# Kernel optimization log

Measured on AMD Instinct MI355X. Metric: run time of the kernel, lower is better.

Reference implementation:

```python
import jax, jax.numpy as jnp
import numpy as np

B, L, D, H, R = 4, 4096, 1024, 16, 30
DK = D // H  # 64
EPS = 1e-12  # torch F.normalize eps


def setup_inputs() -> dict:
    key = jax.random.key(0)
    ks = jax.random.split(key, 16)
    n = lambda k, shp, s=0.02: jax.random.normal(k, shp, jnp.float32) * s
    return {
        "queries": jax.random.normal(ks[0], (B, L, D), jnp.float32),
        "keys": jax.random.normal(ks[1], (B, L, D), jnp.float32),
        "values": jax.random.normal(ks[2], (B, L, D), jnp.float32),
        # linear weights stored as (in, out); equivalent to torch y = x @ W.T + b
        "Wq": n(ks[3], (D, D)), "bq": jnp.zeros((D,), jnp.float32),
        "Wk": n(ks[4], (D, D)), "bk": jnp.zeros((D,), jnp.float32),
        "We": n(ks[5], (H, DK, R), 0.1),
        "Wr": n(ks[6], (H, DK, R), 0.1),
        "Lam": jax.random.uniform(ks[7], (H, R), jnp.float32),
        "Wc": n(ks[8], (2 * R, DK)), "bc": jnp.zeros((DK,), jnp.float32),
        "Wo": n(ks[9], (D, D)), "bo": jnp.zeros((D,), jnp.float32),
    }


def _l2norm(x):
    nrm = jnp.sqrt(jnp.sum(x * x, axis=-1, keepdims=True))
    return x / jnp.maximum(nrm, EPS)


def reference(queries, keys, values, Wq, bq, Wk, bk, We, Wr, Lam, Wc, bc, Wo, bo):
    b, l, _ = queries.shape
    # projections -> [B, H, L, DK]
    q = (queries @ Wq + bq).reshape(b, l, H, DK).transpose(0, 2, 1, 3)
    k = (keys @ Wk + bk).reshape(b, l, H, DK).transpose(0, 2, 1, 3)
    # causal cumulative mean over sequence
    normal = (jnp.arange(l, dtype=jnp.float32) + 1.0)[None, None, :, None]
    q = jnp.cumsum(q, axis=2) / normal
    k = jnp.cumsum(k, axis=2) / normal
    # L2-normalized feature map
    q = _l2norm(q)
    k = _l2norm(k)
    # per-head low-rank projections -> [B, H, L, R]
    escore = jnp.einsum('bhld,hdr->bhlr', q, We)
    rscore = jnp.einsum('bhld,hdr->bhlr', k, Wr)
    score = jnp.concatenate([escore, rscore], axis=-1)  # [B, H, L, 2R]
    out = score @ Wc + bc                                # [B, H, L, DK]
    out = out.transpose(0, 2, 1, 3).reshape(b, l, H * DK)
    out = out @ Wo + bo                                  # [B, L, D]
    # dropout is identity in eval mode
    return (out, escore, rscore, Lam)
```

## Files before the change

### kernel.cpp

```cpp
#include <hip/hip_runtime.h>
#include <hip/hip_bf16.h>

#define BATCH 4
#define LSEQ 4096
#define DMODEL 1024
#define NHEAD 16
#define RDIM 30
#define DKH 64
#define NCHUNK 32
#define CHUNK 128

typedef __attribute__((ext_vector_type(8))) short bf16x8_t;
typedef __attribute__((ext_vector_type(4))) float f32x4_t;

static __device__ __forceinline__ unsigned short f2bf(float f) {
    __hip_bfloat16 h = __float2bfloat16(f);
    unsigned short u;
    __builtin_memcpy(&u, &h, 2);
    return u;
}
static __device__ __forceinline__ float b2f(unsigned short u) {
    unsigned v = ((unsigned)u) << 16;
    float f;
    __builtin_memcpy(&f, &v, 4);
    return f;
}

#define SWAIT_VM8()   { asm volatile("s_waitcnt vmcnt(8)" ::: "memory"); __builtin_amdgcn_sched_barrier(0); }
#define SWAIT_VM0()   { asm volatile("s_waitcnt vmcnt(0)" ::: "memory"); __builtin_amdgcn_sched_barrier(0); }
#define SWAIT_LGKM0() { asm volatile("s_waitcnt lgkmcnt(0)" ::: "memory"); __builtin_amdgcn_sched_barrier(0); }
#define SBARRIER()    { __builtin_amdgcn_s_barrier(); __builtin_amdgcn_sched_barrier(0); }

__global__ void cvt_bf16_kernel(const float* __restrict__ in, unsigned short* __restrict__ out, int n4) {
    int i = blockIdx.x * blockDim.x + threadIdx.x;
    int stride = gridDim.x * blockDim.x;
    for (; i < n4; i += stride) {
        float4 v = ((const float4*)in)[i];
        ushort4 o;
        o.x = f2bf(v.x); o.y = f2bf(v.y); o.z = f2bf(v.z); o.w = f2bf(v.w);
        ((ushort4*)out)[i] = o;
    }
}

__global__ void transpose_cvt_kernel(const float* __restrict__ W, unsigned short* __restrict__ outT,
                                     int Kd, int Nd) {
    __shared__ float tile[32][33];
    int n0 = blockIdx.x * 32, k0 = blockIdx.y * 32;
    int tx = threadIdx.x, ty = threadIdx.y;
    #pragma unroll
    for (int r = ty; r < 32; r += 8)
        tile[r][tx] = W[(size_t)(k0 + r) * Nd + n0 + tx];
    __syncthreads();
    #pragma unroll
    for (int r = ty; r < 32; r += 8)
        outT[(size_t)(n0 + r) * Kd + k0 + tx] = f2bf(tile[tx][r]);
}

__global__ void wpack_kernel(const float* __restrict__ We, const float* __restrict__ Wr,
                             unsigned short* __restrict__ WeP, unsigned short* __restrict__ WrP) {
    int h = blockIdx.x;
    const float* W = blockIdx.y ? Wr : We;
    unsigned short* O = blockIdx.y ? WrP : WeP;
    for (int idx = threadIdx.x; idx < 2048; idx += 256) {
        int col = idx >> 6, k = idx & 63;
        float v = (col < RDIM) ? W[((size_t)h * 64 + k) * RDIM + col] : 0.f;
        O[((size_t)h << 11) + idx] = f2bf(v);
    }
}

__global__ __launch_bounds__(256) void wfold_kernel(
    const float* __restrict__ Wc, const float* __restrict__ Wo,
    unsigned short* __restrict__ WfoldT)
{
    __shared__ float WoT[64][65];
    __shared__ float WcT[64][61];
    const int tid = threadIdx.x;
    const int n0 = blockIdx.x * 64, h = blockIdx.y;
    for (int i = tid; i < 4096; i += 256) {
        int dk = i >> 6, n = i & 63;
        WoT[dk][n] = Wo[(size_t)(h * 64 + dk) * DMODEL + n0 + n];
    }
    for (int i = tid; i < 3840; i += 256) {
        int j = i >> 6, dk = i & 63;
        WcT[dk][j] = Wc[j * 64 + dk];
    }
    __syncthreads();
    #pragma unroll 1
    for (int oo = 0; oo < 16; ++oo) {
        int n = (tid >> 6) + oo * 4;
        int j = tid & 63;
        int jr = (j < 30) ? j : (j >= 32 && j < 62) ? (j - 2) : -1;
        float acc = 0.f;
        if (jr >= 0) {
            #pragma unroll
            for (int dk = 0; dk < 64; ++dk)
                acc = fmaf(WcT[dk][jr], WoT[dk][n], acc);
        }
        WfoldT[(size_t)(n0 + n) * 1024 + h * 64 + j] = f2bf(acc);
    }
}

__global__ void bias2_kernel(const float* __restrict__ Wo, const float* __restrict__ bc,
                             const float* __restrict__ bo, float* __restrict__ bias2) {
    int n = blockIdx.x * 256 + threadIdx.x;
    float a = bo[n];
    for (int d = 0; d < DMODEL; ++d)
        a = fmaf(bc[d & 63], Wo[(size_t)d * DMODEL + n], a);
    bias2[n] = a;
}

#define GBM 256
#define GBN 256
#define GBK 64
#define NTILES 16

template <bool BF16_OUT>
__global__ __launch_bounds__(512, 2) void gemm8_kernel(
    const unsigned short* __restrict__ A,
    const unsigned short* __restrict__ Bt,
    const float* __restrict__ bias,
    void* __restrict__ Cv,
    int M, int N)
{
    __shared__ __align__(16) unsigned short As[2][GBM * GBK];
    __shared__ __align__(16) unsigned short Bs[2][GBM * GBK];
    const int tid = threadIdx.x;
    const int lane = tid & 63;
    const int wid = tid >> 6;
    const int wm = wid >> 2;
    const int wn = wid & 3;
    const int lm = lane & 15;
    const int kb = lane >> 4;

    const int nwg = gridDim.x * gridDim.y;
    const int wg = blockIdx.y * gridDim.x + blockIdx.x;
    const int cpx = nwg >> 3;
    const int swz = (wg & 7) * cpx + (wg >> 3);
    const int bn = swz % gridDim.x;
    const int bm = swz / gridDim.x;

    const unsigned short* Atile = A + (size_t)(bm * GBM) * 1024;
    const unsigned short* Btile = Bt + (size_t)(bn * GBN) * 1024;

    f32x4_t acc[8][4];
    #pragma unroll
    for (int i = 0; i < 8; ++i)
        #pragma unroll
        for (int j = 0; j < 4; ++j)
            acc[i][j] = f32x4_t{0.f, 0.f, 0.f, 0.f};

    auto STAGE = [&](int buf, int kt) {
        #pragma unroll
        for (int seg = 0; seg < 4; ++seg) {
            const int s = (seg << 13) + (tid << 4);
            const int row = s >> 7;
            const int cc = ((s >> 4) & 7) ^ (row & 7);
            const unsigned short* ga = Atile + (size_t)row * 1024 + kt * GBK + cc * 8;
            __builtin_amdgcn_global_load_lds(
                (const __attribute__((address_space(1))) void*)ga,
                (__attribute__((address_space(3))) void*)((char*)&As[buf][0] + (seg << 13) + (wid << 10)),
                16, 0, 0);
            const unsigned short* gb = Btile + (size_t)row * 1024 + kt * GBK + cc * 8;
            __builtin_amdgcn_global_load_lds(
                (const __attribute__((address_space(1))) void*)gb,
                (__attribute__((address_space(3))) void*)((char*)&Bs[buf][0] + (seg << 13) + (wid << 10)),
                16, 0, 0);
        }
    };

    bf16x8_t af[8], bfr[4];
    auto LOADFRAGS = [&](int buf, int ks) {
        #pragma unroll
        for (int i = 0; i < 8; ++i) {
            int row = wm * 128 + i * 16 + lm;
            int cc = (ks * 4 + kb) ^ (row & 7);
            af[i] = *(const bf16x8_t*)((const char*)&As[buf][0] + row * 128 + cc * 16);
        }
        #pragma unroll
        for (int j = 0; j < 4; ++j) {
            int row = wn * 64 + j * 16 + lm;
            int cc = (ks * 4 + kb) ^ (row & 7);
            bfr[j] = *(const bf16x8_t*)((const char*)&Bs[buf][0] + row * 128 + cc * 16);
        }
    };
    auto MFMAC = [&]() {
        __builtin_amdgcn_s_setprio(1);
        #pragma unroll
        for (int i = 0; i < 8; ++i)
            #pragma unroll
            for (int j = 0; j < 4; ++j)
                acc[i][j] = __builtin_amdgcn_mfma_f32_16x16x32_bf16(af[i], bfr[j], acc[i][j], 0, 0, 0);
        __builtin_amdgcn_s_setprio(0);
    };

    STAGE(0, 0);
    STAGE(1, 1);
    SWAIT_VM8();
    SBARRIER();

    int cur = 0;
    for (int t = 0; t < NTILES; ++t) {
        LOADFRAGS(cur, 0);
        MFMAC();
        LOADFRAGS(cur, 1);
        SWAIT_LGKM0();
        SBARRIER();
        if (t + 2 < NTILES) STAGE(cur, t + 2);
        MFMAC();
        if (t + 1 < NTILES) {
            if (t + 2 < NTILES) { SWAIT_VM8(); }
            else                { SWAIT_VM0(); }
            SBARRIER();
        }
        cur ^= 1;
    }

    #pragma unroll
    for (int i = 0; i < 8; ++i) {
        int row = bm * GBM + wm * 128 + i * 16 + (lane >> 4) * 4;
        #pragma unroll
        for (int j = 0; j < 4; ++j) {
            int col = bn * GBN + wn * 64 + j * 16 + lm;
            float bv = bias[col];
            #pragma unroll
            for (int r = 0; r < 4; ++r) {
                float v = acc[i][j][r] + bv;
                if constexpr (BF16_OUT)
                    ((unsigned short*)Cv)[(size_t)(row + r) * N + col] = f2bf(v);
                else
                    ((float*)Cv)[(size_t)(row + r) * N + col] = v;
            }
        }
    }
}

__global__ __launch_bounds__(256) void cumsum_local_kernel(
    unsigned short* __restrict__ Qb, unsigned short* __restrict__ Kb,
    float* __restrict__ partQ, float* __restrict__ partK)
{
    const int tid = threadIdx.x;
    const int c = blockIdx.x;
    const int bz = blockIdx.y;
    const int b = bz >> 1;
    unsigned short* buf = (bz & 1) ? Kb : Qb;
    float* part = (bz & 1) ? partK : partQ;
    size_t base = ((size_t)(b * LSEQ + c * CHUNK)) * DMODEL + tid * 4;
    float rx = 0.f, ry = 0.f, rz = 0.f, rw = 0.f;
    #pragma unroll 4
    for (int i = 0; i < CHUNK; ++i) {
        ushort4 v = *(ushort4*)(buf + base + (size_t)i * DMODEL);
        rx += b2f(v.x); ry += b2f(v.y); rz += b2f(v.z); rw += b2f(v.w);
        ushort4 o;
        o.x = f2bf(rx); o.y = f2bf(ry); o.z = f2bf(rz); o.w = f2bf(rw);
        *(ushort4*)(buf + base + (size_t)i * DMODEL) = o;
    }
    float4 p = make_float4(rx, ry, rz, rw);
    *(float4*)(part + ((size_t)(b * NCHUNK + c)) * DMODEL + tid * 4) = p;
}

__global__ void chunk_offsets_kernel(float* __restrict__ partQ, float* __restrict__ partK)
{
    int t = blockIdx.x * 256 + threadIdx.x;
    float* part = blockIdx.y ? partK : partQ;
    int b = t >> 10, d = t & 1023;
    float run = 0.f;
    #pragma unroll
    for (int c = 0; c < NCHUNK; ++c) {
        size_t idx = ((size_t)(b * NCHUNK + c)) * DMODEL + d;
        float v = part[idx];
        part[idx] = run;
        run += v;
    }
}

__global__ __launch_bounds__(256) void score_kernel(
    const unsigned short* __restrict__ Qc, const unsigned short* __restrict__ Kc,
    const float* __restrict__ partQ, const float* __restrict__ partK,
    const unsigned short* __restrict__ WeP, const unsigned short* __restrict__ WrP,
    float* __restrict__ escore, float* __restrict__ rscore,
    unsigned short* __restrict__ sbf)
{
    __shared__ float n2buf[4][64];
    const int tid = threadIdx.x;
    const int lane = tid & 63;
    const int w = tid >> 6;
    const int lm = lane & 15;
    const int lk = lane >> 4;
    const int c = blockIdx.x;
    const int bh = blockIdx.y;
    const int z = blockIdx.z;
    const int b = bh >> 4, h = bh & 15;
    const unsigned short* X = z ? Kc : Qc;
    const float* part = z ? partK : partQ;
    const unsigned short* WP = z ? WrP : WeP;
    float* eout = z ? rscore : escore;
    const int row0 = c * 256 + w * 64;
    const int co = c * 2 + (w >> 1);

    const float* offp = part + ((size_t)(b * NCHUNK + co)) * DMODEL + h * 64 + lk * 8;
    float o0[8], o1[8];
    {
        float4 a = *(const float4*)(offp);
        float4 bb = *(const float4*)(offp + 4);
        float4 cc = *(const float4*)(offp + 32);
        float4 dd = *(const float4*)(offp + 36);
        o0[0] = a.x; o0[1] = a.y; o0[2] = a.z; o0[3] = a.w;
        o0[4] = bb.x; o0[5] = bb.y; o0[6] = bb.z; o0[7] = bb.w;
        o1[0] = cc.x; o1[1] = cc.y; o1[2] = cc.z; o1[3] = cc.w;
        o1[4] = dd.x; o1[5] = dd.y; o1[6] = dd.z; o1[7] = dd.w;
    }

    const unsigned short* wpb = WP + ((size_t)h << 11) + lm * 64 + lk * 8;
    bf16x8_t b00 = *(const bf16x8_t*)(wpb);
    bf16x8_t b01 = *(const bf16x8_t*)(wpb + 32);
    bf16x8_t b10 = *(const bf16x8_t*)(wpb + 16 * 64);
    bf16x8_t b11 = *(const bf16x8_t*)(wpb + 16 * 64 + 32);

    f32x4_t acc[4][2];
    float n2p[4];
    #pragma unroll
    for (int i = 0; i < 4; ++i) {
        n2p[i] = 0.f;
        acc[i][0] = f32x4_t{0.f, 0.f, 0.f, 0.f};
        acc[i][1] = f32x4_t{0.f, 0.f, 0.f, 0.f};
    }

    const unsigned short* xbase = X + ((size_t)(b * LSEQ + row0 + lm)) * DMODEL + h * 64 + lk * 8;
    #pragma unroll
    for (int i = 0; i < 4; ++i) {
        const unsigned short* xp = xbase + (size_t)(16 * i) * DMODEL;
        bf16x8_t x0 = *(const bf16x8_t*)(xp);
        bf16x8_t x1 = *(const bf16x8_t*)(xp + 32);
        bf16x8_t xa0, xa1;
        #pragma unroll
        for (int j = 0; j < 8; ++j) {
            float xf = b2f((unsigned short)x0[j]) + o0[j];
            n2p[i] = fmaf(xf, xf, n2p[i]);
            xa0[j] = (short)f2bf(xf);
        }
        #pragma unroll
        for (int j = 0; j < 8; ++j) {
            float xf = b2f((unsigned short)x1[j]) + o1[j];
            n2p[i] = fmaf(xf, xf, n2p[i]);
            xa1[j] = (short)f2bf(xf);
        }
        acc[i][0] = __builtin_amdgcn_mfma_f32_16x16x32_bf16(xa0, b00, acc[i][0], 0, 0, 0);
        acc[i][1] = __builtin_amdgcn_mfma_f32_16x16x32_bf16(xa0, b10, acc[i][1], 0, 0, 0);
        acc[i][0] = __builtin_amdgcn_mfma_f32_16x16x32_bf16(xa1, b01, acc[i][0], 0, 0, 0);
        acc[i][1] = __builtin_amdgcn_mfma_f32_16x16x32_bf16(xa1, b11, acc[i][1], 0, 0, 0);
    }

    #pragma unroll
    for (int i = 0; i < 4; ++i) {
        n2p[i] += __shfl_xor(n2p[i], 16);
        n2p[i] += __shfl_xor(n2p[i], 32);
    }
    if (lane < 16) {
        #pragma unroll
        for (int i = 0; i < 4; ++i) n2buf[w][16 * i + lane] = n2p[i];
    }
    __syncthreads();

    #pragma unroll
    for (int i = 0; i < 4; ++i) {
        f32x4_t n2v = *(const f32x4_t*)&n2buf[w][16 * i + lk * 4];
        float inv[4];
        #pragma unroll
        for (int r = 0; r < 4; ++r) {
            int lr = row0 + 16 * i + lk * 4 + r;
            inv[r] = 1.f / fmaxf(sqrtf(n2v[r]), 1e-12f * (float)(lr + 1));
        }
        #pragma unroll
        for (int j = 0; j < 2; ++j) {
            int col = 16 * j + lm;
            #pragma unroll
            for (int r = 0; r < 4; ++r) {
                int lr = row0 + 16 * i + lk * 4 + r;
                float v = acc[i][j][r] * inv[r];
                if (col < RDIM)
                    eout[(((size_t)(b * NHEAD + h)) * LSEQ + lr) * RDIM + col] = v;
                sbf[((size_t)(b * LSEQ + lr)) * 1024 + h * 64 + z * 32 + col] =
                    (col < RDIM) ? f2bf(v) : (unsigned short)0;
            }
        }
    }
}

extern "C" void kernel_launch(void* const* d_in, const int* in_sizes, int n_in,
                              void* d_out, int out_size, void* d_ws, size_t ws_size,
                              hipStream_t stream)
{
    const float* queries = (const float*)d_in[0];
    const float* keys    = (const float*)d_in[1];
    const float* Wq = (const float*)d_in[3];
    const float* bq = (const float*)d_in[4];
    const float* Wk = (const float*)d_in[5];
    const float* bk = (const float*)d_in[6];
    const float* We = (const float*)d_in[7];
    const float* Wr = (const float*)d_in[8];
    const float* Lam = (const float*)d_in[9];
    const float* Wc = (const float*)d_in[10];
    const float* bc = (const float*)d_in[11];
    const float* Wo = (const float*)d_in[12];
    const float* bo = (const float*)d_in[13];

    float* out = (float*)d_out;
    float* escore = out + (size_t)16777216;
    float* rscore = out + (size_t)24641536;
    float* lam_out = out + (size_t)32505856;

    char* ws = (char*)d_ws;
    unsigned short* tmp = (unsigned short*)ws;
    unsigned short* Qb  = (unsigned short*)(ws + 33554432);
    unsigned short* Kb  = (unsigned short*)(ws + 67108864);
    unsigned short* WqT = (unsigned short*)(ws + 100663296);
    unsigned short* WkT = (unsigned short*)(ws + 102760448);
    unsigned short* WfT = (unsigned short*)(ws + 104857600);
    float* bias2 = (float*)(ws + 106954752);
    float* partQ = (float*)(ws + 106958848);
    float* partK = (float*)(ws + 107483136);
    unsigned short* WeP = (unsigned short*)(ws + 108007424);
    unsigned short* WrP = (unsigned short*)(ws + 108072960);

    const int NELEM4 = 16777216 / 4;

    dim3 tb(32, 8);
    transpose_cvt_kernel<<<dim3(32, 32), tb, 0, stream>>>(Wq, WqT, DMODEL, DMODEL);
    transpose_cvt_kernel<<<dim3(32, 32), tb, 0, stream>>>(Wk, WkT, DMODEL, DMODEL);
    wpack_kernel<<<dim3(16, 2), 256, 0, stream>>>(We, Wr, WeP, WrP);
    wfold_kernel<<<dim3(16, 16), 256, 0, stream>>>(Wc, Wo, WfT);
    bias2_kernel<<<4, 256, 0, stream>>>(Wo, bc, bo, bias2);

    cvt_bf16_kernel<<<2048, 256, 0, stream>>>(queries, tmp, NELEM4);
    gemm8_kernel<true><<<dim3(4, 64), 512, 0, stream>>>(tmp, WqT, bq, Qb, 16384, 1024);
    cvt_bf16_kernel<<<2048, 256, 0, stream>>>(keys, tmp, NELEM4);
    gemm8_kernel<true><<<dim3(4, 64), 512, 0, stream>>>(tmp, WkT, bk, Kb, 16384, 1024);

    cumsum_local_kernel<<<dim3(NCHUNK, 8), 256, 0, stream>>>(Qb, Kb, partQ, partK);
    chunk_offsets_kernel<<<dim3(16, 2), 256, 0, stream>>>(partQ, partK);

    score_kernel<<<dim3(16, 64, 2), 256, 0, stream>>>(Qb, Kb, partQ, partK, WeP, WrP,
                                                      escore, rscore, tmp);

    gemm8_kernel<false><<<dim3(4, 64), 512, 0, stream>>>(tmp, WfT, bias2, out, 16384, 1024);

    hipMemcpyAsync(lam_out, Lam, 480 * sizeof(float), hipMemcpyDeviceToDevice, stream);
}
```

Measured before the change: 282.7 us.

## Fuse fp32-to-bf16 conversion into Q/K projection GEMM and batch both via grid z

Removes the standalone cvt_bf16 kernels. The projection GEMM now loads fp32 activations into registers, converts them to bf16 and writes them into the swizzled LDS tile, with the register load software-pipelined one tile ahead. The Q and K projections are merged into a single launch using blockIdx.z. This drops a full bf16 round-trip through HBM and two launches, at the cost of reading A in fp32 (twice the bytes), higher register pressure and VALU conversion work inside the GEMM loop.

```diff
diff --git a/kernel.cpp b/kernel.cpp
--- a/kernel.cpp
+++ b/kernel.cpp
@@ -27,20 +27,10 @@
 }
 
 #define SWAIT_VM8()   { asm volatile("s_waitcnt vmcnt(8)" ::: "memory"); __builtin_amdgcn_sched_barrier(0); }
+#define SWAIT_VM4()   { asm volatile("s_waitcnt vmcnt(4)" ::: "memory"); __builtin_amdgcn_sched_barrier(0); }
 #define SWAIT_VM0()   { asm volatile("s_waitcnt vmcnt(0)" ::: "memory"); __builtin_amdgcn_sched_barrier(0); }
 #define SWAIT_LGKM0() { asm volatile("s_waitcnt lgkmcnt(0)" ::: "memory"); __builtin_amdgcn_sched_barrier(0); }
 #define SBARRIER()    { __builtin_amdgcn_s_barrier(); __builtin_amdgcn_sched_barrier(0); }
-
-__global__ void cvt_bf16_kernel(const float* __restrict__ in, unsigned short* __restrict__ out, int n4) {
-    int i = blockIdx.x * blockDim.x + threadIdx.x;
-    int stride = gridDim.x * blockDim.x;
-    for (; i < n4; i += stride) {
-        float4 v = ((const float4*)in)[i];
-        ushort4 o;
-        o.x = f2bf(v.x); o.y = f2bf(v.y); o.z = f2bf(v.z); o.w = f2bf(v.w);
-        ((ushort4*)out)[i] = o;
-    }
-}
 
 __global__ void transpose_cvt_kernel(const float* __restrict__ W, unsigned short* __restrict__ outT,
                                      int Kd, int Nd) {
@@ -114,13 +104,13 @@
 #define GBK 64
 #define NTILES 16
 
-template <bool BF16_OUT>
+template <bool AF32, bool BF16_OUT>
 __global__ __launch_bounds__(512, 2) void gemm8_kernel(
-    const unsigned short* __restrict__ A,
-    const unsigned short* __restrict__ Bt,
-    const float* __restrict__ bias,
-    void* __restrict__ Cv,
-    int M, int N)
+    const void* __restrict__ Av0, const void* __restrict__ Av1,
+    const unsigned short* __restrict__ Bt0, const unsigned short* __restrict__ Bt1,
+    const float* __restrict__ bias0, const float* __restrict__ bias1,
+    void* __restrict__ Cv0, void* __restrict__ Cv1,
+    int N)
 {
     __shared__ __align__(16) unsigned short As[2][GBM * GBK];
     __shared__ __align__(16) unsigned short Bs[2][GBM * GBK];
@@ -131,6 +121,12 @@
     const int wn = wid & 3;
     const int lm = lane & 15;
     const int kb = lane >> 4;
+    const int z = blockIdx.z;
+
+    const void* Av = z ? Av1 : Av0;
+    const unsigned short* Bt = z ? Bt1 : Bt0;
+    const float* bias = z ? bias1 : bias0;
+    void* Cv = z ? Cv1 : Cv0;
 
     const int nwg = gridDim.x * gridDim.y;
     const int wg = blockIdx.y * gridDim.x + blockIdx.x;
@@ -139,8 +135,11 @@
     const int bn = swz % gridDim.x;
     const int bm = swz / gridDim.x;
 
-    const unsigned short* Atile = A + (size_t)(bm * GBM) * 1024;
     const unsigned short* Btile = Bt + (size_t)(bn * GBN) * 1024;
+    const float* A32_tile = nullptr;
+    const unsigned short* A16_tile = nullptr;
+    if constexpr (AF32) A32_tile = (const float*)Av + (size_t)(bm * GBM) * 1024;
+    else                A16_tile = (const unsigned short*)Av + (size_t)(bm * GBM) * 1024;
 
     f32x4_t acc[8][4];
     #pragma unroll
@@ -149,17 +148,12 @@
         for (int j = 0; j < 4; ++j)
             acc[i][j] = f32x4_t{0.f, 0.f, 0.f, 0.f};
 
-    auto STAGE = [&](int buf, int kt) {
+    auto B_STAGE = [&](int buf, int kt) {
         #pragma unroll
         for (int seg = 0; seg < 4; ++seg) {
             const int s = (seg << 13) + (tid << 4);
             const int row = s >> 7;
             const int cc = ((s >> 4) & 7) ^ (row & 7);
-            const unsigned short* ga = Atile + (size_t)row * 1024 + kt * GBK + cc * 8;
-            __builtin_amdgcn_global_load_lds(
-                (const __attribute__((address_space(1))) void*)ga,
-                (__attribute__((address_space(3))) void*)((char*)&As[buf][0] + (seg << 13) + (wid << 10)),
-                16, 0, 0);
             const unsigned short* gb = Btile + (size_t)row * 1024 + kt * GBK + cc * 8;
             __builtin_amdgcn_global_load_lds(
                 (const __attribute__((address_space(1))) void*)gb,
@@ -167,6 +161,40 @@
                 16, 0, 0);
         }
     };
+    auto A_STAGE16 = [&](int buf, int kt) {
+        #pragma unroll
+        for (int seg = 0; seg < 4; ++seg) {
+            const int s = (seg << 13) + (tid << 4);
+            const int row = s >> 7;
+            const int cc = ((s >> 4) & 7) ^ (row & 7);
+            const unsigned short* ga = A16_tile + (size_t)row * 1024 + kt * GBK + cc * 8;
+            __builtin_amdgcn_global_load_lds(
+                (const __attribute__((address_space(1))) void*)ga,
+                (__attribute__((address_space(3))) void*)((char*)&As[buf][0] + (seg << 13) + (wid << 10)),
+                16, 0, 0);
+        }
+    };
+    float4 areg[8];
+    auto A_ISSUE = [&](int kt) {
+        #pragma unroll
+        for (int p = 0; p < 8; ++p) {
+            int q = p * 512 + tid;
+            int row = q >> 4, kq = q & 15;
+            areg[p] = *(const float4*)(A32_tile + (size_t)row * 1024 + kt * GBK + kq * 4);
+        }
+    };
+    auto A_WRITE = [&](int buf) {
+        #pragma unroll
+        for (int p = 0; p < 8; ++p) {
+            int q = p * 512 + tid;
+            int row = q >> 4, kq = q & 15;
+            ushort4 pk;
+            pk.x = f2bf(areg[p].x); pk.y = f2bf(areg[p].y);
+            pk.z = f2bf(areg[p].z); pk.w = f2bf(areg[p].w);
+            int cc = (kq >> 1) ^ (row & 7);
+            *(ushort4*)((char*)&As[buf][0] + row * 128 + (cc << 4) + (kq & 1) * 8) = pk;
+        }
+    };
 
     bf16x8_t af[8], bfr[4];
     auto LOADFRAGS = [&](int buf, int ks) {
@@ -193,10 +221,24 @@
         __builtin_amdgcn_s_setprio(0);
     };
 
-    STAGE(0, 0);
-    STAGE(1, 1);
-    SWAIT_VM8();
-    SBARRIER();
+    if constexpr (AF32) {
+        B_STAGE(0, 0);
+        A_ISSUE(0);
+        SWAIT_VM0();
+        A_WRITE(0);
+        B_STAGE(1, 1);
+        A_ISSUE(1);
+        SWAIT_LGKM0();
+        SBARRIER();
+    } else {
+        A_STAGE16(0, 0);
+        B_STAGE(0, 0);
+        __builtin_amdgcn_sched_barrier(0);
+        A_STAGE16(1, 1);
+        B_STAGE(1, 1);
+        SWAIT_VM8();
+        SBARRIER();
+    }
 
     int cur = 0;
     for (int t = 0; t < NTILES; ++t) {
@@ -205,12 +247,24 @@
         LOADFRAGS(cur, 1);
         SWAIT_LGKM0();
         SBARRIER();
-        if (t + 2 < NTILES) STAGE(cur, t + 2);
-        MFMAC();
-        if (t + 1 < NTILES) {
-            if (t + 2 < NTILES) { SWAIT_VM8(); }
-            else                { SWAIT_VM0(); }
-            SBARRIER();
+        if constexpr (AF32) {
+            if (t + 2 < NTILES) B_STAGE(cur, t + 2);
+            if (t + 1 < NTILES) {
+                if (t + 2 < NTILES) { SWAIT_VM4(); }
+                else                { SWAIT_VM0(); }
+                A_WRITE(cur ^ 1);
+                if (t + 2 < NTILES) A_ISSUE(t + 2);
+            }
+            MFMAC();
+            if (t + 1 < NTILES) { SWAIT_LGKM0(); SBARRIER(); }
+        } else {
+            if (t + 2 < NTILES) { A_STAGE16(cur, t + 2); B_STAGE(cur, t + 2); }
+            MFMAC();
+            if (t + 1 < NTILES) {
+                if (t + 2 < NTILES) { SWAIT_VM8(); }
+                else                { SWAIT_VM0(); }
+                SBARRIER();
+            }
         }
         cur ^= 1;
     }
@@ -410,7 +464,7 @@
     float* lam_out = out + (size_t)32505856;
 
     char* ws = (char*)d_ws;
-    unsigned short* tmp = (unsigned short*)ws;
+    unsigned short* sbf = (unsigned short*)ws;
     unsigned short* Qb  = (unsigned short*)(ws + 33554432);
     unsigned short* Kb  = (unsigned short*)(ws + 67108864);
     unsigned short* WqT = (unsigned short*)(ws + 100663296);
@@ -422,8 +476,6 @@
     unsigned short* WeP = (unsigned short*)(ws + 108007424);
     unsigned short* WrP = (unsigned short*)(ws + 108072960);
 
-    const int NELEM4 = 16777216 / 4;
-
     dim3 tb(32, 8);
     transpose_cvt_kernel<<<dim3(32, 32), tb, 0, stream>>>(Wq, WqT, DMODEL, DMODEL);
     transpose_cvt_kernel<<<dim3(32, 32), tb, 0, stream>>>(Wk, WkT, DMODEL, DMODEL);
@@ -431,18 +483,17 @@
     wfold_kernel<<<dim3(16, 16), 256, 0, stream>>>(Wc, Wo, WfT);
     bias2_kernel<<<4, 256, 0, stream>>>(Wo, bc, bo, bias2);
 
-    cvt_bf16_kernel<<<2048, 256, 0, stream>>>(queries, tmp, NELEM4);
-    gemm8_kernel<true><<<dim3(4, 64), 512, 0, stream>>>(tmp, WqT, bq, Qb, 16384, 1024);
-    cvt_bf16_kernel<<<2048, 256, 0, stream>>>(keys, tmp, NELEM4);
-    gemm8_kernel<true><<<dim3(4, 64), 512, 0, stream>>>(tmp, WkT, bk, Kb, 16384, 1024);
+    gemm8_kernel<true, true><<<dim3(4, 64, 2), 512, 0, stream>>>(
+        queries, keys, WqT, WkT, bq, bk, Qb, Kb, 1024);
 
     cumsum_local_kernel<<<dim3(NCHUNK, 8), 256, 0, stream>>>(Qb, Kb, partQ, partK);
     chunk_offsets_kernel<<<dim3(16, 2), 256, 0, stream>>>(partQ, partK);
 
     score_kernel<<<dim3(16, 64, 2), 256, 0, stream>>>(Qb, Kb, partQ, partK, WeP, WrP,
-                                                      escore, rscore, tmp);
-
-    gemm8_kernel<false><<<dim3(4, 64), 512, 0, stream>>>(tmp, WfT, bias2, out, 16384, 1024);
+                                                      escore, rscore, sbf);
+
+    gemm8_kernel<false, false><<<dim3(4, 64, 1), 512, 0, stream>>>(
+        sbf, sbf, WfT, WfT, bias2, bias2, out, out, 1024);
 
     hipMemcpyAsync(lam_out, Lam, 480 * sizeof(float), hipMemcpyDeviceToDevice, stream);
 }
```

Measured after the change: 277.1 us. 1.02x faster.

## Restructure GEMM into half-K phased pipeline with four LDS slots

Applied to the files above, without the earlier changes.

Rewrites the bf16 GEMM main loop so each 64-wide K tile is split into two 32-wide halves held in separate LDS slots, with staging of future halves interleaved between fine-grained load/MFMA phases. A fragments are loaded per M-half, which reduces live fragment registers. The swizzle changes to match 64-byte rows. The aim is better overlap of global-to-LDS loads with MFMA work, at the cost of more barriers per tile.

```diff
diff --git a/kernel.cpp b/kernel.cpp
--- a/kernel.cpp
+++ b/kernel.cpp
@@ -27,9 +27,11 @@
 }
 
 #define SWAIT_VM8()   { asm volatile("s_waitcnt vmcnt(8)" ::: "memory"); __builtin_amdgcn_sched_barrier(0); }
+#define SWAIT_VM4()   { asm volatile("s_waitcnt vmcnt(4)" ::: "memory"); __builtin_amdgcn_sched_barrier(0); }
 #define SWAIT_VM0()   { asm volatile("s_waitcnt vmcnt(0)" ::: "memory"); __builtin_amdgcn_sched_barrier(0); }
 #define SWAIT_LGKM0() { asm volatile("s_waitcnt lgkmcnt(0)" ::: "memory"); __builtin_amdgcn_sched_barrier(0); }
 #define SBARRIER()    { __builtin_amdgcn_s_barrier(); __builtin_amdgcn_sched_barrier(0); }
+#define NOSTG ((void)0)
 
 __global__ void cvt_bf16_kernel(const float* __restrict__ in, unsigned short* __restrict__ out, int n4) {
     int i = blockIdx.x * blockDim.x + threadIdx.x;
@@ -111,19 +113,26 @@
 
 #define GBM 256
 #define GBN 256
-#define GBK 64
 #define NTILES 16
 
+#define BASE_A(buf,kh) ((((buf)*2+(kh))*16384))
+#define BASE_B(buf,kh) ((65536 + ((buf)*2+(kh))*16384))
+
+#define PH_ODD(ab, bb, stg) \
+    LDB(bb); LDA(ab, 0); stg; \
+    SBARRIER(); SWAIT_LGKM0(); MF(0); SBARRIER();
+#define PH_EVEN(ab, stg, wait) \
+    LDA(ab, 1); stg; \
+    SBARRIER(); SWAIT_LGKM0(); MF(1); wait; SBARRIER();
+
 template <bool BF16_OUT>
-__global__ __launch_bounds__(512, 2) void gemm8_kernel(
+__global__ __launch_bounds__(512, 2) void gemm8p_kernel(
     const unsigned short* __restrict__ A,
     const unsigned short* __restrict__ Bt,
     const float* __restrict__ bias,
-    void* __restrict__ Cv,
-    int M, int N)
-{
-    __shared__ __align__(16) unsigned short As[2][GBM * GBK];
-    __shared__ __align__(16) unsigned short Bs[2][GBM * GBK];
+    void* __restrict__ Cv, int N)
+{
+    __shared__ __align__(16) char smem[131072];
     const int tid = threadIdx.x;
     const int lane = tid & 63;
     const int wid = tid >> 6;
@@ -149,71 +158,74 @@
         for (int j = 0; j < 4; ++j)
             acc[i][j] = f32x4_t{0.f, 0.f, 0.f, 0.f};
 
-    auto STAGE = [&](int buf, int kt) {
-        #pragma unroll
-        for (int seg = 0; seg < 4; ++seg) {
-            const int s = (seg << 13) + (tid << 4);
-            const int row = s >> 7;
-            const int cc = ((s >> 4) & 7) ^ (row & 7);
-            const unsigned short* ga = Atile + (size_t)row * 1024 + kt * GBK + cc * 8;
+    auto STG = [&](const unsigned short* gsrc, int ldsbase, int kt, int kh) {
+        #pragma unroll
+        for (int g = 0; g < 2; ++g) {
+            const int d = (g << 13) + (tid << 4);
+            const int row = d >> 6;
+            const int ks = ((d >> 4) & 3) ^ ((row >> 1) & 3);
+            const unsigned short* p = gsrc + (size_t)row * 1024 + kt * 64 + kh * 32 + ks * 8;
             __builtin_amdgcn_global_load_lds(
-                (const __attribute__((address_space(1))) void*)ga,
-                (__attribute__((address_space(3))) void*)((char*)&As[buf][0] + (seg << 13) + (wid << 10)),
+                (const __attribute__((address_space(1))) void*)p,
+                (__attribute__((address_space(3))) void*)(smem + ldsbase + d),
                 16, 0, 0);
-            const unsigned short* gb = Btile + (size_t)row * 1024 + kt * GBK + cc * 8;
-            __builtin_amdgcn_global_load_lds(
-                (const __attribute__((address_space(1))) void*)gb,
-                (__attribute__((address_space(3))) void*)((char*)&Bs[buf][0] + (seg << 13) + (wid << 10)),
-                16, 0, 0);
         }
     };
 
-    bf16x8_t af[8], bfr[4];
-    auto LOADFRAGS = [&](int buf, int ks) {
-        #pragma unroll
-        for (int i = 0; i < 8; ++i) {
-            int row = wm * 128 + i * 16 + lm;
-            int cc = (ks * 4 + kb) ^ (row & 7);
-            af[i] = *(const bf16x8_t*)((const char*)&As[buf][0] + row * 128 + cc * 16);
-        }
+    bf16x8_t af[4], bfr[4];
+    auto LDA = [&](int base, int mh) {
+        #pragma unroll
+        for (int i2 = 0; i2 < 4; ++i2) {
+            const int row = wm * 128 + mh * 64 + i2 * 16 + lm;
+            const int s = kb ^ ((row >> 1) & 3);
+            af[i2] = *(const bf16x8_t*)(smem + base + row * 64 + (s << 4));
+        }
+    };
+    auto LDB = [&](int base) {
         #pragma unroll
         for (int j = 0; j < 4; ++j) {
-            int row = wn * 64 + j * 16 + lm;
-            int cc = (ks * 4 + kb) ^ (row & 7);
-            bfr[j] = *(const bf16x8_t*)((const char*)&Bs[buf][0] + row * 128 + cc * 16);
+            const int row = wn * 64 + j * 16 + lm;
+            const int s = kb ^ ((row >> 1) & 3);
+            bfr[j] = *(const bf16x8_t*)(smem + base + row * 64 + (s << 4));
         }
     };
-    auto MFMAC = [&]() {
+    auto MF = [&](int mh) {
         __builtin_amdgcn_s_setprio(1);
         #pragma unroll
-        for (int i = 0; i < 8; ++i)
+        for (int i2 = 0; i2 < 4; ++i2)
             #pragma unroll
             for (int j = 0; j < 4; ++j)
-                acc[i][j] = __builtin_amdgcn_mfma_f32_16x16x32_bf16(af[i], bfr[j], acc[i][j], 0, 0, 0);
+                acc[mh * 4 + i2][j] =
+                    __builtin_amdgcn_mfma_f32_16x16x32_bf16(af[i2], bfr[j], acc[mh * 4 + i2][j], 0, 0, 0);
         __builtin_amdgcn_s_setprio(0);
     };
 
-    STAGE(0, 0);
-    STAGE(1, 1);
+    STG(Atile, BASE_A(0, 0), 0, 0); STG(Btile, BASE_B(0, 0), 0, 0);
+    STG(Atile, BASE_A(0, 1), 0, 1); STG(Btile, BASE_B(0, 1), 0, 1);
+    STG(Atile, BASE_A(1, 0), 1, 0); STG(Btile, BASE_B(1, 0), 1, 0);
     SWAIT_VM8();
     SBARRIER();
 
-    int cur = 0;
-    for (int t = 0; t < NTILES; ++t) {
-        LOADFRAGS(cur, 0);
-        MFMAC();
-        LOADFRAGS(cur, 1);
-        SWAIT_LGKM0();
-        SBARRIER();
-        if (t + 2 < NTILES) STAGE(cur, t + 2);
-        MFMAC();
-        if (t + 1 < NTILES) {
-            if (t + 2 < NTILES) { SWAIT_VM8(); }
-            else                { SWAIT_VM0(); }
-            SBARRIER();
-        }
-        cur ^= 1;
-    }
+    #pragma unroll 1
+    for (int i = 0; i < 7; ++i) {
+        const int t1 = 2 * i + 1, t2 = 2 * i + 2, t3 = 2 * i + 3;
+        PH_ODD (BASE_A(0, 0), BASE_B(0, 0), STG(Atile, BASE_A(1, 1), t1, 1));
+        PH_EVEN(BASE_A(0, 0),               STG(Btile, BASE_B(1, 1), t1, 1), SWAIT_VM8());
+        PH_ODD (BASE_A(0, 1), BASE_B(0, 1), STG(Atile, BASE_A(0, 0), t2, 0));
+        PH_EVEN(BASE_A(0, 1),               STG(Btile, BASE_B(0, 0), t2, 0), SWAIT_VM8());
+        PH_ODD (BASE_A(1, 0), BASE_B(1, 0), STG(Atile, BASE_A(0, 1), t2, 1));
+        PH_EVEN(BASE_A(1, 0),               STG(Btile, BASE_B(0, 1), t2, 1), SWAIT_VM8());
+        PH_ODD (BASE_A(1, 1), BASE_B(1, 1), STG(Atile, BASE_A(1, 0), t3, 0));
+        PH_EVEN(BASE_A(1, 1),               STG(Btile, BASE_B(1, 0), t3, 0), SWAIT_VM8());
+    }
+    PH_ODD (BASE_A(0, 0), BASE_B(0, 0), STG(Atile, BASE_A(1, 1), 15, 1));
+    PH_EVEN(BASE_A(0, 0),               STG(Btile, BASE_B(1, 1), 15, 1), SWAIT_VM8());
+    PH_ODD (BASE_A(0, 1), BASE_B(0, 1), NOSTG);
+    PH_EVEN(BASE_A(0, 1),               NOSTG, SWAIT_VM4());
+    PH_ODD (BASE_A(1, 0), BASE_B(1, 0), NOSTG);
+    PH_EVEN(BASE_A(1, 0),               NOSTG, SWAIT_VM0());
+    PH_ODD (BASE_A(1, 1), BASE_B(1, 1), NOSTG);
+    PH_EVEN(BASE_A(1, 1),               NOSTG, NOSTG);
 
     #pragma unroll
     for (int i = 0; i < 8; ++i) {
@@ -432,9 +444,9 @@
     bias2_kernel<<<4, 256, 0, stream>>>(Wo, bc, bo, bias2);
 
     cvt_bf16_kernel<<<2048, 256, 0, stream>>>(queries, tmp, NELEM4);
-    gemm8_kernel<true><<<dim3(4, 64), 512, 0, stream>>>(tmp, WqT, bq, Qb, 16384, 1024);
+    gemm8p_kernel<true><<<dim3(4, 64), 512, 0, stream>>>(tmp, WqT, bq, Qb, 1024);
     cvt_bf16_kernel<<<2048, 256, 0, stream>>>(keys, tmp, NELEM4);
-    gemm8_kernel<true><<<dim3(4, 64), 512, 0, stream>>>(tmp, WkT, bk, Kb, 16384, 1024);
+    gemm8p_kernel<true><<<dim3(4, 64), 512, 0, stream>>>(tmp, WkT, bk, Kb, 1024);
 
     cumsum_local_kernel<<<dim3(NCHUNK, 8), 256, 0, stream>>>(Qb, Kb, partQ, partK);
     chunk_offsets_kernel<<<dim3(16, 2), 256, 0, stream>>>(partQ, partK);
@@ -442,7 +454,7 @@
     score_kernel<<<dim3(16, 64, 2), 256, 0, stream>>>(Qb, Kb, partQ, partK, WeP, WrP,
                                                       escore, rscore, tmp);
 
-    gemm8_kernel<false><<<dim3(4, 64), 512, 0, stream>>>(tmp, WfT, bias2, out, 16384, 1024);
+    gemm8p_kernel<false><<<dim3(4, 64), 512, 0, stream>>>(tmp, WfT, bias2, out, 1024);
 
     hipMemcpyAsync(lam_out, Lam, 480 * sizeof(float), hipMemcpyDeviceToDevice, stream);
 }
```

Result: no change. 278.9 us (-1.4%).
